# Kernel tuning notes

Measured on AMD Instinct MI355X. Metric: run time of the kernel, lower is better.

The kernel has to match this reference:

```python
import jax, jax.numpy as jnp
import numpy as np

BS, LX, LY, H, MD = 16, 1024, 1024, 512, 512


def setup_inputs() -> dict:
    key = jax.random.key(0)
    ks = jax.random.split(key, 8)
    x = jax.random.normal(ks[0], (BS, LX, H), dtype=jnp.float32)
    y = jax.random.normal(ks[1], (BS, LY, H), dtype=jnp.float32)
    y_mask = jax.random.bernoulli(ks[2], 0.2, (BS, LY))  # True = masked
    s1 = 1.0 / np.sqrt(H)
    W1 = jax.random.uniform(ks[3], (MD, H), jnp.float32, -s1, s1)
    b1 = jax.random.uniform(ks[4], (MD,), jnp.float32, -s1, s1)
    W2 = jax.random.uniform(ks[5], (MD, H), jnp.float32, -s1, s1)
    b2 = jax.random.uniform(ks[6], (MD,), jnp.float32, -s1, s1)
    s2 = 1.0 / np.sqrt(MD)
    k7, k8 = jax.random.split(ks[7])
    w_o = jax.random.uniform(k7, (MD,), jnp.float32, -s2, s2)
    b_o = jax.random.uniform(k8, (), jnp.float32, -s2, s2)
    return {"x": x, "y": y, "y_mask": y_mask, "W1": W1, "b1": b1,
            "W2": W2, "b2": b2, "w_o": w_o, "b_o": b_o}


def reference(x, y, y_mask, W1, b1, W2, b2, w_o, b_o):
    # Projections: [B,L,MD]
    x_proj = jax.nn.relu(jnp.einsum('blh,mh->blm', x, W1) + b1)
    y_proj = jax.nn.relu(jnp.einsum('blh,mh->blm', y, W2) + b2)
    # o_liner is linear, so o_liner(x_i + y_j) = w_o.x_i + w_o.y_j + b_o
    sx = x_proj @ w_o  # [B,Lx]
    sy = y_proj @ w_o  # [B,Ly]
    scores = sx[:, :, None] + sy[:, None, :] + b_o  # [B,Lx,Ly]
    scores = jnp.where(y_mask[:, None, :], jnp.float32(-1e7), scores)
    alpha = jax.nn.softmax(scores, axis=-1)  # softmax over len_y
    return alpha
```

## Files before the change

### kernel.cpp

```cpp
#include <hip/hip_runtime.h>
#include <hip/hip_bf16.h>

#define BS 16
#define LX 1024
#define LY 1024
#define H 512
#define MD 512
#define RY (BS * LY)

typedef __attribute__((ext_vector_type(8))) __bf16 bf16x8;
typedef __attribute__((ext_vector_type(4))) __bf16 bf16x4;
typedef __attribute__((ext_vector_type(4))) float floatx4;

#define BK 32
#define LDS_STRIDE 40

__global__ __launch_bounds__(256) void gemm_sy(const float* __restrict__ Y,
                                               const float* __restrict__ W2,
                                               const float* __restrict__ b2,
                                               const float* __restrict__ wo,
                                               float* __restrict__ sy) {
    __shared__ __align__(16) __bf16 As[128 * LDS_STRIDE];
    __shared__ __align__(16) __bf16 Bs[128 * LDS_STRIDE];

    const int tid  = threadIdx.x;
    const int lane = tid & 63;
    const int wave = tid >> 6;
    const int wm = wave >> 1;
    const int wn = wave & 1;
    const int nt = blockIdx.x;
    const int mt = blockIdx.y;

    const int la = lane & 15;
    const int qa = lane >> 4;

    floatx4 acc[4][4] = {};

    const int row_m_base = mt * 128;
    const int row_n_base = nt * 128;

    for (int k0 = 0; k0 < H; k0 += BK) {
        __syncthreads();
        #pragma unroll
        for (int c = 0; c < 4; ++c) {
            const int f   = c * 256 + tid;
            const int row = f >> 3;
            const int kq  = f & 7;
            const float4 av = *(const float4*)(Y  + (size_t)(row_m_base + row) * H + k0 + kq * 4);
            const float4 bv = *(const float4*)(W2 + (size_t)(row_n_base + row) * H + k0 + kq * 4);
            bf16x4 ap = { (__bf16)av.x, (__bf16)av.y, (__bf16)av.z, (__bf16)av.w };
            bf16x4 bp = { (__bf16)bv.x, (__bf16)bv.y, (__bf16)bv.z, (__bf16)bv.w };
            *(bf16x4*)&As[row * LDS_STRIDE + kq * 4] = ap;
            *(bf16x4*)&Bs[row * LDS_STRIDE + kq * 4] = bp;
        }
        __syncthreads();

        bf16x8 afr[4], bfr[4];
        #pragma unroll
        for (int mf = 0; mf < 4; ++mf)
            afr[mf] = *(const bf16x8*)&As[(wm * 64 + mf * 16 + la) * LDS_STRIDE + qa * 8];
        #pragma unroll
        for (int nf = 0; nf < 4; ++nf)
            bfr[nf] = *(const bf16x8*)&Bs[(wn * 64 + nf * 16 + la) * LDS_STRIDE + qa * 8];

        #pragma unroll
        for (int mf = 0; mf < 4; ++mf)
            #pragma unroll
            for (int nf = 0; nf < 4; ++nf)
                acc[mf][nf] = __builtin_amdgcn_mfma_f32_16x16x32_bf16(afr[mf], bfr[nf], acc[mf][nf], 0, 0, 0);
    }

    #pragma unroll
    for (int mf = 0; mf < 4; ++mf) {
        #pragma unroll
        for (int reg = 0; reg < 4; ++reg) {
            float s = 0.f;
            #pragma unroll
            for (int nf = 0; nf < 4; ++nf) {
                const int n = row_n_base + wn * 64 + nf * 16 + la;
                float v = acc[mf][nf][reg] + b2[n];
                v = fmaxf(v, 0.f);
                s += v * wo[n];
            }
            s += __shfl_xor(s, 1);
            s += __shfl_xor(s, 2);
            s += __shfl_xor(s, 4);
            s += __shfl_xor(s, 8);
            if (la == 0) {
                const int m = row_m_base + wm * 64 + mf * 16 + qa * 4 + reg;
                atomicAdd(&sy[m], s);
            }
        }
    }
}

__global__ __launch_bounds__(256) void softmax_p(const float* __restrict__ sy,
                                                 const int* __restrict__ mask,
                                                 float* __restrict__ p) {
    const int b = blockIdx.x;
    const int tid = threadIdx.x;
    __shared__ float red[8];

    float vals[4];
    int   ms[4];
    float mx = -INFINITY;
    #pragma unroll
    for (int c = 0; c < 4; ++c) {
        const int j = c * 256 + tid;
        vals[c] = sy[b * LY + j];
        ms[c]   = mask[b * LY + j];
        if (!ms[c]) mx = fmaxf(mx, vals[c]);
    }
    #pragma unroll
    for (int off = 1; off < 64; off <<= 1) mx = fmaxf(mx, __shfl_xor(mx, off));
    if ((tid & 63) == 0) red[tid >> 6] = mx;
    __syncthreads();
    mx = fmaxf(fmaxf(red[0], red[1]), fmaxf(red[2], red[3]));

    float e[4];
    float sum = 0.f;
    #pragma unroll
    for (int c = 0; c < 4; ++c) {
        e[c] = ms[c] ? 0.f : __expf(vals[c] - mx);
        sum += e[c];
    }
    #pragma unroll
    for (int off = 1; off < 64; off <<= 1) sum += __shfl_xor(sum, off);
    if ((tid & 63) == 0) red[4 + (tid >> 6)] = sum;
    __syncthreads();
    sum = red[4] + red[5] + red[6] + red[7];
    const float inv = 1.0f / sum;

    #pragma unroll
    for (int c = 0; c < 4; ++c)
        p[b * LY + c * 256 + tid] = e[c] * inv;
}

__global__ __launch_bounds__(256) void bcast(const float* __restrict__ p,
                                             float4* __restrict__ out) {
    const int tid = threadIdx.x;
    const long base_row = (long)blockIdx.x * 8;
    const int b = (int)(base_row >> 10);
    const float4 v = *(const float4*)(p + b * LY + tid * 4);
    float4* o = out + base_row * (LY / 4) + tid;
    #pragma unroll
    for (int r = 0; r < 8; ++r) o[r * (LY / 4)] = v;
}

extern "C" void kernel_launch(void* const* d_in, const int* in_sizes, int n_in,
                              void* d_out, int out_size, void* d_ws, size_t ws_size,
                              hipStream_t stream) {
    const float* y  = (const float*)d_in[1];
    const int*   ym = (const int*)  d_in[2];
    const float* W2 = (const float*)d_in[5];
    const float* b2 = (const float*)d_in[6];
    const float* wo = (const float*)d_in[7];

    float* sy = (float*)d_ws;
    float* p  = sy + RY;

    hipMemsetAsync(sy, 0, RY * sizeof(float), stream);

    dim3 gg(MD / 128, RY / 128);
    gemm_sy<<<gg, 256, 0, stream>>>(y, W2, b2, wo, sy);
    softmax_p<<<BS, 256, 0, stream>>>(sy, ym, p);
    bcast<<<(BS * LX) / 8, 256, 0, stream>>>(p, (float4*)d_out);
}
```

Before: 153.3 us.

## Pre-convert inputs to bf16, direct-to-LDS loads, and partial-sum buffers instead of atomics

A new prep kernel converts Y and W2 to bf16 once. The GEMM then stages tiles into LDS with global_load_lds 16-byte transfers instead of converting fp32 in registers. The GEMM tile becomes 64x128 with a K step of 64. Instead of atomicAdd into a zeroed buffer, each N-slice writes its own partial row sums, which the softmax kernel adds up, so the memset goes away. This costs an extra full pass over Y in the conversion, and the unpadded LDS layout may cause bank conflicts on fragment reads.

```diff
diff --git a/kernel.cpp b/kernel.cpp
--- a/kernel.cpp
+++ b/kernel.cpp
@@ -9,75 +9,97 @@
 #define RY (BS * LY)
 
 typedef __attribute__((ext_vector_type(8))) __bf16 bf16x8;
-typedef __attribute__((ext_vector_type(4))) __bf16 bf16x4;
 typedef __attribute__((ext_vector_type(4))) float floatx4;
 
-#define BK 32
-#define LDS_STRIDE 40
+__device__ __forceinline__ void load_lds16(const __bf16* g, __bf16* l) {
+    __builtin_amdgcn_global_load_lds(
+        (const __attribute__((address_space(1))) void*)g,
+        (__attribute__((address_space(3))) void*)l,
+        16, 0, 0);
+}
 
-__global__ __launch_bounds__(256) void gemm_sy(const float* __restrict__ Y,
-                                               const float* __restrict__ W2,
+__global__ __launch_bounds__(256) void prep(const float* __restrict__ Y,
+                                            const float* __restrict__ W2,
+                                            __bf16* __restrict__ yb,
+                                            __bf16* __restrict__ wb) {
+    const long i = (long)blockIdx.x * 256 + threadIdx.x;
+    const float* src; __bf16* dst; long off;
+    if (blockIdx.x < 4096) { src = Y;  dst = yb; off = i; }
+    else                   { src = W2; dst = wb; off = i - 4096L * 256; }
+    const float4 a = *(const float4*)(src + off * 8);
+    const float4 b = *(const float4*)(src + off * 8 + 4);
+    bf16x8 v = { (__bf16)a.x, (__bf16)a.y, (__bf16)a.z, (__bf16)a.w,
+                 (__bf16)b.x, (__bf16)b.y, (__bf16)b.z, (__bf16)b.w };
+    *(bf16x8*)(dst + off * 8) = v;
+}
+
+#define BM 64
+#define BN 128
+#define BKT 64
+__global__ __launch_bounds__(256) void gemm_sy(const __bf16* __restrict__ yb,
+                                               const __bf16* __restrict__ wb,
                                                const float* __restrict__ b2,
                                                const float* __restrict__ wo,
-                                               float* __restrict__ sy) {
-    __shared__ __align__(16) __bf16 As[128 * LDS_STRIDE];
-    __shared__ __align__(16) __bf16 Bs[128 * LDS_STRIDE];
+                                               float* __restrict__ part) {
+    __shared__ __align__(16) __bf16 As[BM * BKT];
+    __shared__ __align__(16) __bf16 Bs[BN * BKT];
 
     const int tid  = threadIdx.x;
     const int lane = tid & 63;
     const int wave = tid >> 6;
     const int wm = wave >> 1;
     const int wn = wave & 1;
+    const int la = lane & 15;
+    const int qa = lane >> 4;
     const int nt = blockIdx.x;
     const int mt = blockIdx.y;
+    const int m0 = mt * BM, n0 = nt * BN;
 
-    const int la = lane & 15;
-    const int qa = lane >> 4;
+    const int lrow = lane >> 3;
+    const int lcol = (lane & 7) * 8;
 
-    floatx4 acc[4][4] = {};
+    floatx4 acc[2][4] = {};
 
-    const int row_m_base = mt * 128;
-    const int row_n_base = nt * 128;
-
-    for (int k0 = 0; k0 < H; k0 += BK) {
+    for (int k0 = 0; k0 < H; k0 += BKT) {
         __syncthreads();
         #pragma unroll
-        for (int c = 0; c < 4; ++c) {
-            const int f   = c * 256 + tid;
-            const int row = f >> 3;
-            const int kq  = f & 7;
-            const float4 av = *(const float4*)(Y  + (size_t)(row_m_base + row) * H + k0 + kq * 4);
-            const float4 bv = *(const float4*)(W2 + (size_t)(row_n_base + row) * H + k0 + kq * 4);
-            bf16x4 ap = { (__bf16)av.x, (__bf16)av.y, (__bf16)av.z, (__bf16)av.w };
-            bf16x4 bp = { (__bf16)bv.x, (__bf16)bv.y, (__bf16)bv.z, (__bf16)bv.w };
-            *(bf16x4*)&As[row * LDS_STRIDE + kq * 4] = ap;
-            *(bf16x4*)&Bs[row * LDS_STRIDE + kq * 4] = bp;
+        for (int r = 0; r < 2; ++r) {
+            const int rb = r * 32 + wave * 8;
+            load_lds16(yb + (size_t)(m0 + rb + lrow) * H + k0 + lcol, &As[rb * BKT]);
+        }
+        #pragma unroll
+        for (int r = 0; r < 4; ++r) {
+            const int rb = r * 32 + wave * 8;
+            load_lds16(wb + (size_t)(n0 + rb + lrow) * H + k0 + lcol, &Bs[rb * BKT]);
         }
         __syncthreads();
 
-        bf16x8 afr[4], bfr[4];
         #pragma unroll
-        for (int mf = 0; mf < 4; ++mf)
-            afr[mf] = *(const bf16x8*)&As[(wm * 64 + mf * 16 + la) * LDS_STRIDE + qa * 8];
-        #pragma unroll
-        for (int nf = 0; nf < 4; ++nf)
-            bfr[nf] = *(const bf16x8*)&Bs[(wn * 64 + nf * 16 + la) * LDS_STRIDE + qa * 8];
-
-        #pragma unroll
-        for (int mf = 0; mf < 4; ++mf)
+        for (int kh = 0; kh < 2; ++kh) {
+            bf16x8 afr[2], bfr[4];
+            #pragma unroll
+            for (int mf = 0; mf < 2; ++mf)
+                afr[mf] = *(const bf16x8*)&As[(wm * 32 + mf * 16 + la) * BKT + kh * 32 + qa * 8];
             #pragma unroll
             for (int nf = 0; nf < 4; ++nf)
-                acc[mf][nf] = __builtin_amdgcn_mfma_f32_16x16x32_bf16(afr[mf], bfr[nf], acc[mf][nf], 0, 0, 0);
+                bfr[nf] = *(const bf16x8*)&Bs[(wn * 64 + nf * 16 + la) * BKT + kh * 32 + qa * 8];
+            #pragma unroll
+            for (int mf = 0; mf < 2; ++mf)
+                #pragma unroll
+                for (int nf = 0; nf < 4; ++nf)
+                    acc[mf][nf] = __builtin_amdgcn_mfma_f32_16x16x32_bf16(afr[mf], bfr[nf], acc[mf][nf], 0, 0, 0);
+        }
     }
 
+    const int slice = nt * 2 + wn;
     #pragma unroll
-    for (int mf = 0; mf < 4; ++mf) {
+    for (int mf = 0; mf < 2; ++mf) {
         #pragma unroll
         for (int reg = 0; reg < 4; ++reg) {
             float s = 0.f;
             #pragma unroll
             for (int nf = 0; nf < 4; ++nf) {
-                const int n = row_n_base + wn * 64 + nf * 16 + la;
+                const int n = n0 + wn * 64 + nf * 16 + la;
                 float v = acc[mf][nf][reg] + b2[n];
                 v = fmaxf(v, 0.f);
                 s += v * wo[n];
@@ -87,14 +109,14 @@
             s += __shfl_xor(s, 4);
             s += __shfl_xor(s, 8);
             if (la == 0) {
-                const int m = row_m_base + wm * 64 + mf * 16 + qa * 4 + reg;
-                atomicAdd(&sy[m], s);
+                const int m = m0 + wm * 32 + mf * 16 + qa * 4 + reg;
+                part[(size_t)slice * RY + m] = s;
             }
         }
     }
 }
 
-__global__ __launch_bounds__(256) void softmax_p(const float* __restrict__ sy,
+__global__ __launch_bounds__(256) void softmax_p(const float* __restrict__ part,
                                                  const int* __restrict__ mask,
                                                  float* __restrict__ p) {
     const int b = blockIdx.x;
@@ -107,9 +129,12 @@
     #pragma unroll
     for (int c = 0; c < 4; ++c) {
         const int j = c * 256 + tid;
-        vals[c] = sy[b * LY + j];
+        float v = 0.f;
+        #pragma unroll
+        for (int t = 0; t < 8; ++t) v += part[t * RY + b * LY + j];
+        vals[c] = v;
         ms[c]   = mask[b * LY + j];
-        if (!ms[c]) mx = fmaxf(mx, vals[c]);
+        if (!ms[c]) mx = fmaxf(mx, v);
     }
     #pragma unroll
     for (int off = 1; off < 64; off <<= 1) mx = fmaxf(mx, __shfl_xor(mx, off));
@@ -156,13 +181,15 @@
     const float* b2 = (const float*)d_in[6];
     const float* wo = (const float*)d_in[7];
 
-    float* sy = (float*)d_ws;
-    float* p  = sy + RY;
+    char* ws = (char*)d_ws;
+    __bf16* yb   = (__bf16*)ws;
+    __bf16* wb   = (__bf16*)(ws + (size_t)RY * H * 2);
+    float*  part = (float*)(ws + (size_t)RY * H * 2 + (size_t)MD * H * 2);
+    float*  p    = part + 8 * RY;
 
-    hipMemsetAsync(sy, 0, RY * sizeof(float), stream);
-
-    dim3 gg(MD / 128, RY / 128);
-    gemm_sy<<<gg, 256, 0, stream>>>(y, W2, b2, wo, sy);
-    softmax_p<<<BS, 256, 0, stream>>>(sy, ym, p);
+    prep<<<4096 + 128, 256, 0, stream>>>(y, W2, yb, wb);
+    dim3 gg(MD / BN, RY / BM);
+    gemm_sy<<<gg, 256, 0, stream>>>(yb, wb, b2, wo, part);
+    softmax_p<<<BS, 256, 0, stream>>>(part, ym, p);
     bcast<<<(BS * LX) / 8, 256, 0, stream>>>(p, (float4*)d_out);
 }
```

After: 151.9 us. No clear change (-0.9%).
